# Kernel tuning notes

Hardware: AMD Instinct MI355X
Metric: run time of the kernel (lower is better)

The kernel has to match this reference:

```python
import jax, jax.numpy as jnp
import numpy as np

B, S, F, H, L = 128, 1024, 256, 256, 2


def setup_inputs() -> dict:
    key = jax.random.key(0)
    ks = jax.random.split(key, 6)
    x = jax.random.normal(ks[0], (B, S, F), dtype=jnp.float32)
    # nn.Linear default init ~ U(-1/sqrt(fan_in), 1/sqrt(fan_in)); use scaled normal for simplicity
    s_in = 1.0 / np.sqrt(F)
    s_h = 1.0 / np.sqrt(H)
    W_ih = jax.random.normal(ks[1], (L, 3 * H, F), dtype=jnp.float32) * s_in
    b_ih = jax.random.normal(ks[2], (L, 3 * H), dtype=jnp.float32) * s_in
    W_hh = jax.random.normal(ks[3], (L, 3 * H, H), dtype=jnp.float32) * s_h
    b_hh = jax.random.normal(ks[4], (L, 3 * H), dtype=jnp.float32) * s_h
    fw = jnp.ones((1, 1, F), dtype=jnp.float32)   # features_weighting (init: ones)
    tw = jnp.ones((1, S, 1), dtype=jnp.float32)   # times_weighting (init: ones)
    return {"x": x, "fw": fw, "tw": tw, "W_ih": W_ih, "b_ih": b_ih, "W_hh": W_hh, "b_hh": b_hh}


def _lstm_forward(x, fw, tw, W_ih, b_ih, W_hh, b_hh):
    batch = x.shape[0]
    xw = x * fw * tw  # (B,S,F)
    h0 = jnp.zeros((L, batch, H), dtype=x.dtype)
    c0 = jnp.zeros((L, batch, H), dtype=x.dtype)

    def step(carry, x_t):
        hs, cs = carry  # each (L,B,H)
        inp = x_t
        new_hs, new_cs = [], []
        for l in range(L):
            gates = inp @ W_ih[l].T + b_ih[l] + hs[l] @ W_hh[l].T + b_hh[l]  # (B,3H)
            i_g, g_g, o_g = jnp.split(gates, 3, axis=1)
            f = jax.nn.sigmoid(cs[l])            # NOTE: forget gate = sigmoid(c_prev) per source
            c = f * cs[l] + jax.nn.sigmoid(i_g) * jnp.tanh(g_g)
            h = jax.nn.sigmoid(o_g) * jnp.tanh(c)
            new_hs.append(h)
            new_cs.append(c)
            inp = h
        return (jnp.stack(new_hs), jnp.stack(new_cs)), inp

    (hs, cs), outs = jax.lax.scan(step, (h0, c0), jnp.swapaxes(xw, 0, 1))
    outputs = jnp.swapaxes(outs, 0, 1)  # (B,S,H)
    return outputs, hs, cs


def reference(x, fw, tw, W_ih, b_ih, W_hh, b_hh):
    return _lstm_forward(x, fw, tw, W_ih, b_ih, W_hh, b_hh)
```

## Files before the change

kernel.cpp:

```cpp
#include <hip/hip_runtime.h>
#include <math.h>

#define B_ 128
#define S_ 1024
#define F_ 256
#define H_ 256
#define G3 768
#define BGROUPS 4
#define NBLK 256
#define NTHR 64
#define H0_DEPTH 8
#define H1_DEPTH 2

#define SLAB_U64 4096
#define H0_U64 (H0_DEPTH * BGROUPS * SLAB_U64)
#define H1_U64 (H1_DEPTH * BGROUPS * SLAB_U64)
#define WS_ZERO_BYTES (4096 + (size_t)(H0_U64 + H1_U64) * 8)

typedef __bf16 bf16x8 __attribute__((ext_vector_type(8)));
typedef float f32x4 __attribute__((ext_vector_type(4)));
typedef unsigned short us8 __attribute__((ext_vector_type(8)));
typedef unsigned long long u64;

__device__ __forceinline__ float sigf(float v) { return 1.0f / (1.0f + __expf(-v)); }
__device__ __forceinline__ float tanh_fast(float v) {
    return __builtin_fmaf(2.0f, sigf(2.0f * v), -1.0f);
}
__device__ __forceinline__ unsigned short f2bf(float f) {
    unsigned u = __builtin_bit_cast(unsigned, f);
    return (unsigned short)((u + 0x7fffu + ((u >> 16) & 1u)) >> 16);
}
__device__ __forceinline__ f32x4 MF(bf16x8 a, bf16x8 b, f32x4 c) {
    return __builtin_amdgcn_mfma_f32_16x16x32_bf16(a, b, c, 0, 0, 0);
}
__device__ __forceinline__ u64 aload(const u64* p) {
    return __hip_atomic_load(p, __ATOMIC_RELAXED, __HIP_MEMORY_SCOPE_AGENT);
}
__device__ __forceinline__ void astore(u64* p, u64 v) {
    __hip_atomic_store(p, v, __ATOMIC_RELAXED, __HIP_MEMORY_SCOPE_AGENT);
}
__device__ __forceinline__ unsigned aload32(const unsigned* p) {
    return __hip_atomic_load(p, __ATOMIC_RELAXED, __HIP_MEMORY_SCOPE_AGENT);
}
__device__ __forceinline__ void astore32(unsigned* p, unsigned v) {
    __hip_atomic_store(p, v, __ATOMIC_RELAXED, __HIP_MEMORY_SCOPE_AGENT);
}

__device__ __forceinline__ void loadq(const u64* rdb, u64* q) {
    #pragma unroll
    for (int pl = 0; pl < 8; ++pl)
        #pragma unroll
        for (int jp = 0; jp < 4; ++jp)
            q[pl * 4 + jp] = aload(rdb + pl * 256 + jp * 16);
}
__device__ __forceinline__ bool tagok(const u64* q, unsigned tag) {
    unsigned acc = 0;
    #pragma unroll
    for (int i = 0; i < 32; ++i) {
        acc |= ((unsigned)q[i] ^ tag) & 0xFFFFu;
        acc |= ((unsigned)(q[i] >> 32) ^ tag) & 0xFFFFu;
    }
    return acc == 0u;
}
__device__ __forceinline__ bf16x8 unpk(const u64* qq) {
    us8 u;
    u[0] = (unsigned short)(qq[0] >> 16); u[1] = (unsigned short)(qq[0] >> 48);
    u[2] = (unsigned short)(qq[1] >> 16); u[3] = (unsigned short)(qq[1] >> 48);
    u[4] = (unsigned short)(qq[2] >> 16); u[5] = (unsigned short)(qq[2] >> 48);
    u[6] = (unsigned short)(qq[3] >> 16); u[7] = (unsigned short)(qq[3] >> 48);
    return __builtin_bit_cast(bf16x8, u);
}

__global__ __launch_bounds__(NTHR)
void lstm_w1(const float* __restrict__ x,
             const float* __restrict__ fw,
             const float* __restrict__ tw,
             const float* __restrict__ Wih,
             const float* __restrict__ bih,
             const float* __restrict__ Whh,
             const float* __restrict__ bhh,
             float* __restrict__ out,
             void* __restrict__ ws)
{
    __shared__ unsigned short sW[3 * 16 * 64 * 8];

    unsigned* prog = (unsigned*)ws;
    u64* h0buf = (u64*)((char*)ws + 4096);
    u64* h1buf = h0buf + H0_U64;
    float* outputs = out;
    float* hs = out + (size_t)B_ * S_ * H_;
    float* cs = hs + (size_t)2 * B_ * H_;

    const int bid   = blockIdx.x;
    const int lane  = threadIdx.x;
    const int ntw   = bid & 1;
    const int uh    = (bid >> 1) & 1;
    const int bg    = (bid >> 2) & 3;
    const int ug    = (bid >> 4) & 7;
    const int layer = (bid >> 7) & 1;

    const float* Wih_l = Wih + (size_t)layer * G3 * F_;
    const float* Whh_l = Whh + (size_t)layer * G3 * H_;

    for (int idx = lane; idx < 3 * 16 * 64; idx += NTHR) {
        const int l  = idx & 63;
        const int kt = (idx >> 6) & 15;
        const int g  = idx >> 10;
        const int grow = g * H_ + ug * 32 + uh * 16 + (l & 15);
        const int k = kt * 32 + (l >> 4) * 8;
        float4 a, b;
        if (k < 256) {
            const float* s = Wih_l + (size_t)grow * F_ + k;
            a = *(const float4*)s; b = *(const float4*)(s + 4);
            if (layer == 0) {
                const float4 wa = *(const float4*)(fw + k);
                const float4 wb = *(const float4*)(fw + k + 4);
                a.x *= wa.x; a.y *= wa.y; a.z *= wa.z; a.w *= wa.w;
                b.x *= wb.x; b.y *= wb.y; b.z *= wb.z; b.w *= wb.w;
            }
        } else {
            const float* s = Whh_l + (size_t)grow * H_ + (k - 256);
            a = *(const float4*)s; b = *(const float4*)(s + 4);
        }
        us8 w;
        w[0] = f2bf(a.x); w[1] = f2bf(a.y); w[2] = f2bf(a.z); w[3] = f2bf(a.w);
        w[4] = f2bf(b.x); w[5] = f2bf(b.y); w[6] = f2bf(b.z); w[7] = f2bf(b.w);
        *(us8*)&sW[(size_t)idx * 8] = w;
    }
    __syncthreads();

    float bia[3][4];
    #pragma unroll
    for (int r = 0; r < 4; ++r) {
        const int gu = ug * 32 + uh * 16 + (lane >> 4) * 4 + r;
        #pragma unroll
        for (int s = 0; s < 3; ++s)
            bia[s][r] = bih[layer * G3 + s * H_ + gu] + bhh[layer * G3 + s * H_ + gu];
    }

    const int ul0  = uh * 16 + (lane >> 4) * 4;
    const int hg0  = ug * 32 + ul0;
    const int bcol = bg * 32 + ntw * 16 + (lane & 15);
    const size_t wofs = (size_t)ntw * 2048 + (size_t)ug * 256
                      + (size_t)(uh * 2 + ((lane >> 4) >> 1)) * 64
                      + (size_t)(((lane >> 4) & 1) * 2) * 16 + (lane & 15);
    const size_t rofs = (size_t)ntw * 2048 + (size_t)(lane >> 4) * 64 + (lane & 15);
    const int dom = bg * 2 + ntw;

    float c_reg[4] = {0.f, 0.f, 0.f, 0.f};

    #define WAf(g, kt) (*(const bf16x8*)&sW[(size_t)(((g) * 16 + (kt)) * 64 + lane) * 8])

    if (layer == 0) {
        float4 xf[16];
        #pragma unroll
        for (int kt = 0; kt < 8; ++kt) {
            const float* s = x + ((size_t)bcol * S_ + 0) * F_ + kt * 32 + (lane >> 4) * 8;
            xf[2 * kt] = *(const float4*)s; xf[2 * kt + 1] = *(const float4*)(s + 4);
        }
        float twc = tw[0], twn = tw[1];

        for (int p = 0; p < S_; ++p) {
            const u64* rdb = h0buf + (size_t)(((p - 1) & 7) * BGROUPS + bg) * SLAB_U64 + rofs;
            u64 q[32];
            loadq(rdb, q);

            bf16x8 xb[8];
            #pragma unroll
            for (int kt = 0; kt < 8; ++kt) {
                const float4 a = xf[2 * kt], b = xf[2 * kt + 1];
                us8 w;
                w[0] = f2bf(a.x); w[1] = f2bf(a.y); w[2] = f2bf(a.z); w[3] = f2bf(a.w);
                w[4] = f2bf(b.x); w[5] = f2bf(b.y); w[6] = f2bf(b.z); w[7] = f2bf(b.w);
                xb[kt] = __builtin_bit_cast(bf16x8, w);
            }
            if (p + 1 < S_) {
                #pragma unroll
                for (int kt = 0; kt < 8; ++kt) {
                    const float* s = x + ((size_t)bcol * S_ + (p + 1)) * F_
                                   + kt * 32 + (lane >> 4) * 8;
                    xf[2 * kt] = *(const float4*)s; xf[2 * kt + 1] = *(const float4*)(s + 4);
                }
            }

            f32x4 ai = {0.f, 0.f, 0.f, 0.f}, ag = ai, ao = ai;
            #pragma unroll
            for (int kt = 0; kt < 8; ++kt) {
                ai = MF(WAf(0, kt), xb[kt], ai);
                ag = MF(WAf(1, kt), xb[kt], ag);
                ao = MF(WAf(2, kt), xb[kt], ao);
            }
            #pragma unroll
            for (int r = 0; r < 4; ++r) {
                ai[r] *= twc; ag[r] *= twc; ao[r] *= twc;
            }

            while (!__all(tagok(q, (unsigned)p))) loadq(rdb, q);
            #pragma unroll
            for (int pl = 0; pl < 8; ++pl) {
                const bf16x8 hb = unpk(&q[pl * 4]);
                ai = MF(WAf(0, 8 + pl), hb, ai);
                ag = MF(WAf(1, 8 + pl), hb, ag);
                ao = MF(WAf(2, 8 + pl), hb, ao);
            }

            if (p >= H0_DEPTH) {
                const unsigned need = (unsigned)(p - (H0_DEPTH - 1));
                bool ok;
                do {
                    const unsigned pv = (lane < 16)
                        ? aload32(&prog[dom * 16 + lane]) : need;
                    ok = __all((int)(pv >= need));
                } while (!ok);
            }

            u64* wb = h0buf + (size_t)((p & 7) * BGROUPS + bg) * SLAB_U64 + wofs;
            const unsigned tagv = (unsigned)(p + 1);
            float hnv[4], cnv[4];
            unsigned er[4];
            #pragma unroll
            for (int r = 0; r < 4; ++r) {
                const float gi = ai[r] + bia[0][r];
                const float gg = ag[r] + bia[1][r];
                const float go = ao[r] + bia[2][r];
                const float cp = c_reg[r];
                const float fg = sigf(cp);
                const float cn = fg * cp + sigf(gi) * tanh_fast(gg);
                const float hn = sigf(go) * tanh_fast(cn);
                c_reg[r] = cn; hnv[r] = hn; cnv[r] = cn;
                er[r] = ((unsigned)f2bf(hn) << 16) | tagv;
            }
            astore(wb,      er[0] | ((u64)er[1] << 32));
            astore(wb + 16, er[2] | ((u64)er[3] << 32));

            if (p == S_ - 1) {
                *(float4*)(hs + (size_t)bcol * H_ + hg0) =
                    make_float4(hnv[0], hnv[1], hnv[2], hnv[3]);
                *(float4*)(cs + (size_t)bcol * H_ + hg0) =
                    make_float4(cnv[0], cnv[1], cnv[2], cnv[3]);
            }
            twc = twn;
            if (p + 2 < S_) twn = tw[p + 2];
        }
    } else {
        for (int p = 1; p <= S_; ++p) {
            const int t = p - 1;
            const u64* rd0 = h0buf + (size_t)(((p - 1) & 7) * BGROUPS + bg) * SLAB_U64 + rofs;
            const u64* rd1 = h1buf + (size_t)(((p - 2) & 1) * BGROUPS + bg) * SLAB_U64 + rofs;
            u64 q0[32], q1[32];
            loadq(rd0, q0);
            loadq(rd1, q1);

            while (!__all(tagok(q0, (unsigned)p))) loadq(rd0, q0);
            if (lane == 0)
                astore32(&prog[dom * 16 + ug * 2 + uh], (unsigned)p);

            f32x4 ai = {0.f, 0.f, 0.f, 0.f}, ag = ai, ao = ai;
            #pragma unroll
            for (int pl = 0; pl < 8; ++pl) {
                const bf16x8 hb = unpk(&q0[pl * 4]);
                ai = MF(WAf(0, pl), hb, ai);
                ag = MF(WAf(1, pl), hb, ag);
                ao = MF(WAf(2, pl), hb, ao);
            }

            while (!__all(tagok(q1, (unsigned)(p - 1)))) loadq(rd1, q1);
            #pragma unroll
            for (int pl = 0; pl < 8; ++pl) {
                const bf16x8 hb = unpk(&q1[pl * 4]);
                ai = MF(WAf(0, 8 + pl), hb, ai);
                ag = MF(WAf(1, 8 + pl), hb, ag);
                ao = MF(WAf(2, 8 + pl), hb, ao);
            }

            u64* wb = h1buf + (size_t)(((p - 1) & 1) * BGROUPS + bg) * SLAB_U64 + wofs;
            const unsigned tagv = (unsigned)p;
            float hnv[4], cnv[4];
            unsigned er[4];
            #pragma unroll
            for (int r = 0; r < 4; ++r) {
                const float gi = ai[r] + bia[0][r];
                const float gg = ag[r] + bia[1][r];
                const float go = ao[r] + bia[2][r];
                const float cp = c_reg[r];
                const float fg = sigf(cp);
                const float cn = fg * cp + sigf(gi) * tanh_fast(gg);
                const float hn = sigf(go) * tanh_fast(cn);
                c_reg[r] = cn; hnv[r] = hn; cnv[r] = cn;
                er[r] = ((unsigned)f2bf(hn) << 16) | tagv;
            }
            astore(wb,      er[0] | ((u64)er[1] << 32));
            astore(wb + 16, er[2] | ((u64)er[3] << 32));

            *(float4*)(outputs + ((size_t)bcol * S_ + t) * H_ + hg0) =
                make_float4(hnv[0], hnv[1], hnv[2], hnv[3]);
            if (p == S_) {
                *(float4*)(hs + (size_t)B_ * H_ + (size_t)bcol * H_ + hg0) =
                    make_float4(hnv[0], hnv[1], hnv[2], hnv[3]);
                *(float4*)(cs + (size_t)B_ * H_ + (size_t)bcol * H_ + hg0) =
                    make_float4(cnv[0], cnv[1], cnv[2], cnv[3]);
            }
        }
    }
}

extern "C" void kernel_launch(void* const* d_in, const int* in_sizes, int n_in,
                              void* d_out, int out_size, void* d_ws, size_t ws_size,
                              hipStream_t stream) {
    const float* x   = (const float*)d_in[0];
    const float* fw  = (const float*)d_in[1];
    const float* tw  = (const float*)d_in[2];
    const float* Wih = (const float*)d_in[3];
    const float* bih = (const float*)d_in[4];
    const float* Whh = (const float*)d_in[5];
    const float* bhh = (const float*)d_in[6];
    float* out = (float*)d_out;

    hipMemsetAsync(d_ws, 0, WS_ZERO_BYTES, stream);

    void* kargs[] = { (void*)&x, (void*)&fw, (void*)&tw, (void*)&Wih, (void*)&bih,
                      (void*)&Whh, (void*)&bhh, (void*)&out, (void*)&d_ws };
    hipError_t e = hipLaunchCooperativeKernel((const void*)lstm_w1,
                                              dim3(NBLK), dim3(NTHR),
                                              kargs, 0, stream);
    if (e != hipSuccess) {
        lstm_w1<<<dim3(NBLK), dim3(NTHR), 0, stream>>>(
            x, fw, tw, Wih, bih, Whh, bhh, out, d_ws);
    }
}
```

Measured before the change: 4.004 ms.

## Halve block count; each block handles two batch groups with interleaved pipelines

The kernel now launches half as many single-wave blocks, and each block processes two batch groups. It interleaves their recurrent steps so one group's work can hide the other's wait on the handoff buffers. The next step's h-buffer reads are also prefetched right after the current step's stores, and s_sleep is added inside the spin loops to ease polling pressure. In exchange, each wave carries more register state (two copies of q and x) and does serial work per step, which could lengthen the critical path of the recurrence.

```diff
diff --git a/kernel.cpp b/kernel.cpp
--- a/kernel.cpp
+++ b/kernel.cpp
@@ -7,7 +7,7 @@
 #define H_ 256
 #define G3 768
 #define BGROUPS 4
-#define NBLK 256
+#define NBLK 128
 #define NTHR 64
 #define H0_DEPTH 8
 #define H1_DEPTH 2
@@ -71,8 +71,8 @@
     return __builtin_bit_cast(bf16x8, u);
 }
 
-__global__ __launch_bounds__(NTHR)
-void lstm_w1(const float* __restrict__ x,
+__global__ __launch_bounds__(NTHR, 1)
+void lstm_w2(const float* __restrict__ x,
              const float* __restrict__ fw,
              const float* __restrict__ tw,
              const float* __restrict__ Wih,
@@ -93,11 +93,11 @@
 
     const int bid   = blockIdx.x;
     const int lane  = threadIdx.x;
-    const int ntw   = bid & 1;
-    const int uh    = (bid >> 1) & 1;
-    const int bg    = (bid >> 2) & 3;
-    const int ug    = (bid >> 4) & 7;
-    const int layer = (bid >> 7) & 1;
+    const int bgp   = bid & 1;
+    const int nt    = (bid >> 1) & 1;
+    const int uh    = (bid >> 2) & 1;
+    const int ug    = (bid >> 3) & 7;
+    const int layer = (bid >> 6) & 1;
 
     const float* Wih_l = Wih + (size_t)layer * G3 * F_;
     const float* Whh_l = Whh + (size_t)layer * G3 * H_;
@@ -138,167 +138,200 @@
             bia[s][r] = bih[layer * G3 + s * H_ + gu] + bhh[layer * G3 + s * H_ + gu];
     }
 
-    const int ul0  = uh * 16 + (lane >> 4) * 4;
-    const int hg0  = ug * 32 + ul0;
-    const int bcol = bg * 32 + ntw * 16 + (lane & 15);
-    const size_t wofs = (size_t)ntw * 2048 + (size_t)ug * 256
+    const int ul0 = uh * 16 + (lane >> 4) * 4;
+    const int hg0 = ug * 32 + ul0;
+    const size_t wofs = (size_t)nt * 2048 + (size_t)ug * 256
                       + (size_t)(uh * 2 + ((lane >> 4) >> 1)) * 64
                       + (size_t)(((lane >> 4) & 1) * 2) * 16 + (lane & 15);
-    const size_t rofs = (size_t)ntw * 2048 + (size_t)(lane >> 4) * 64 + (lane & 15);
-    const int dom = bg * 2 + ntw;
-
-    float c_reg[4] = {0.f, 0.f, 0.f, 0.f};
+    const size_t rofs = (size_t)nt * 2048 + (size_t)(lane >> 4) * 64 + (lane & 15);
+
+    int bg[2], bcol[2], dom[2];
+    #pragma unroll
+    for (int c = 0; c < 2; ++c) {
+        bg[c]   = bgp * 2 + c;
+        bcol[c] = bg[c] * 32 + nt * 16 + (lane & 15);
+        dom[c]  = bg[c] * 2 + nt;
+    }
+
+    float c_reg[2][4] = {{0.f,0.f,0.f,0.f},{0.f,0.f,0.f,0.f}};
 
     #define WAf(g, kt) (*(const bf16x8*)&sW[(size_t)(((g) * 16 + (kt)) * 64 + lane) * 8])
 
     if (layer == 0) {
-        float4 xf[16];
+        float4 xr[2][16];
+        u64 q[2][32];
         #pragma unroll
-        for (int kt = 0; kt < 8; ++kt) {
-            const float* s = x + ((size_t)bcol * S_ + 0) * F_ + kt * 32 + (lane >> 4) * 8;
-            xf[2 * kt] = *(const float4*)s; xf[2 * kt + 1] = *(const float4*)(s + 4);
-        }
-        float twc = tw[0], twn = tw[1];
-
-        for (int p = 0; p < S_; ++p) {
-            const u64* rdb = h0buf + (size_t)(((p - 1) & 7) * BGROUPS + bg) * SLAB_U64 + rofs;
-            u64 q[32];
-            loadq(rdb, q);
-
-            bf16x8 xb[8];
+        for (int c = 0; c < 2; ++c) {
             #pragma unroll
             for (int kt = 0; kt < 8; ++kt) {
-                const float4 a = xf[2 * kt], b = xf[2 * kt + 1];
-                us8 w;
-                w[0] = f2bf(a.x); w[1] = f2bf(a.y); w[2] = f2bf(a.z); w[3] = f2bf(a.w);
-                w[4] = f2bf(b.x); w[5] = f2bf(b.y); w[6] = f2bf(b.z); w[7] = f2bf(b.w);
-                xb[kt] = __builtin_bit_cast(bf16x8, w);
+                const float* s = x + ((size_t)bcol[c] * S_) * F_ + kt * 32 + (lane >> 4) * 8;
+                xr[c][2 * kt] = *(const float4*)s;
+                xr[c][2 * kt + 1] = *(const float4*)(s + 4);
             }
-            if (p + 1 < S_) {
+            loadq(h0buf + (size_t)(7 * BGROUPS + bg[c]) * SLAB_U64 + rofs, q[c]);
+        }
+
+        for (int p = 0; p < S_; ++p) {
+            const float twc = tw[p];
+            #pragma unroll
+            for (int c = 0; c < 2; ++c) {
+                bf16x8 xb[8];
                 #pragma unroll
                 for (int kt = 0; kt < 8; ++kt) {
-                    const float* s = x + ((size_t)bcol * S_ + (p + 1)) * F_
-                                   + kt * 32 + (lane >> 4) * 8;
-                    xf[2 * kt] = *(const float4*)s; xf[2 * kt + 1] = *(const float4*)(s + 4);
+                    const float4 a = xr[c][2 * kt], b = xr[c][2 * kt + 1];
+                    us8 w;
+                    w[0] = f2bf(a.x); w[1] = f2bf(a.y); w[2] = f2bf(a.z); w[3] = f2bf(a.w);
+                    w[4] = f2bf(b.x); w[5] = f2bf(b.y); w[6] = f2bf(b.z); w[7] = f2bf(b.w);
+                    xb[kt] = __builtin_bit_cast(bf16x8, w);
+                }
+                f32x4 ai = {0.f, 0.f, 0.f, 0.f}, ag = ai, ao = ai;
+                #pragma unroll
+                for (int kt = 0; kt < 8; ++kt) {
+                    ai = MF(WAf(0, kt), xb[kt], ai);
+                    ag = MF(WAf(1, kt), xb[kt], ag);
+                    ao = MF(WAf(2, kt), xb[kt], ao);
+                }
+                #pragma unroll
+                for (int r = 0; r < 4; ++r) { ai[r] *= twc; ag[r] *= twc; ao[r] *= twc; }
+
+                const u64* rdb = h0buf
+                    + (size_t)(((p - 1) & 7) * BGROUPS + bg[c]) * SLAB_U64 + rofs;
+                while (!__all(tagok(q[c], (unsigned)p))) {
+                    __builtin_amdgcn_s_sleep(1);
+                    loadq(rdb, q[c]);
+                }
+                #pragma unroll
+                for (int pl = 0; pl < 8; ++pl) {
+                    const bf16x8 hb = unpk(&q[c][pl * 4]);
+                    ai = MF(WAf(0, 8 + pl), hb, ai);
+                    ag = MF(WAf(1, 8 + pl), hb, ag);
+                    ao = MF(WAf(2, 8 + pl), hb, ao);
+                }
+
+                if (p >= H0_DEPTH) {
+                    const unsigned need = (unsigned)(p - (H0_DEPTH - 1));
+                    bool ok;
+                    do {
+                        const unsigned pv = (lane < 16)
+                            ? aload32(&prog[dom[c] * 16 + lane]) : need;
+                        ok = __all((int)(pv >= need));
+                    } while (!ok);
+                }
+
+                u64* wb = h0buf + (size_t)((p & 7) * BGROUPS + bg[c]) * SLAB_U64 + wofs;
+                const unsigned tagv = (unsigned)(p + 1);
+                float hnv[4], cnv[4];
+                unsigned er[4];
+                #pragma unroll
+                for (int r = 0; r < 4; ++r) {
+                    const float gi = ai[r] + bia[0][r];
+                    const float gg = ag[r] + bia[1][r];
+                    const float go = ao[r] + bia[2][r];
+                    const float cp = c_reg[c][r];
+                    const float fg = sigf(cp);
+                    const float cn = fg * cp + sigf(gi) * tanh_fast(gg);
+                    const float hn = sigf(go) * tanh_fast(cn);
+                    c_reg[c][r] = cn; hnv[r] = hn; cnv[r] = cn;
+                    er[r] = ((unsigned)f2bf(hn) << 16) | tagv;
+                }
+                astore(wb,      er[0] | ((u64)er[1] << 32));
+                astore(wb + 16, er[2] | ((u64)er[3] << 32));
+
+                if (p == S_ - 1) {
+                    *(float4*)(hs + (size_t)bcol[c] * H_ + hg0) =
+                        make_float4(hnv[0], hnv[1], hnv[2], hnv[3]);
+                    *(float4*)(cs + (size_t)bcol[c] * H_ + hg0) =
+                        make_float4(cnv[0], cnv[1], cnv[2], cnv[3]);
+                } else {
+                    #pragma unroll
+                    for (int kt = 0; kt < 8; ++kt) {
+                        const float* s = x + ((size_t)bcol[c] * S_ + (p + 1)) * F_
+                                       + kt * 32 + (lane >> 4) * 8;
+                        xr[c][2 * kt] = *(const float4*)s;
+                        xr[c][2 * kt + 1] = *(const float4*)(s + 4);
+                    }
+                    loadq(h0buf + (size_t)((p & 7) * BGROUPS + bg[c]) * SLAB_U64 + rofs,
+                          q[c]);
                 }
             }
-
-            f32x4 ai = {0.f, 0.f, 0.f, 0.f}, ag = ai, ao = ai;
-            #pragma unroll
-            for (int kt = 0; kt < 8; ++kt) {
-                ai = MF(WAf(0, kt), xb[kt], ai);
-                ag = MF(WAf(1, kt), xb[kt], ag);
-                ao = MF(WAf(2, kt), xb[kt], ao);
-            }
-            #pragma unroll
-            for (int r = 0; r < 4; ++r) {
-                ai[r] *= twc; ag[r] *= twc; ao[r] *= twc;
-            }
-
-            while (!__all(tagok(q, (unsigned)p))) loadq(rdb, q);
-            #pragma unroll
-            for (int pl = 0; pl < 8; ++pl) {
-                const bf16x8 hb = unpk(&q[pl * 4]);
-                ai = MF(WAf(0, 8 + pl), hb, ai);
-                ag = MF(WAf(1, 8 + pl), hb, ag);
-                ao = MF(WAf(2, 8 + pl), hb, ao);
-            }
-
-            if (p >= H0_DEPTH) {
-                const unsigned need = (unsigned)(p - (H0_DEPTH - 1));
-                bool ok;
-                do {
-                    const unsigned pv = (lane < 16)
-                        ? aload32(&prog[dom * 16 + lane]) : need;
-                    ok = __all((int)(pv >= need));
-                } while (!ok);
-            }
-
-            u64* wb = h0buf + (size_t)((p & 7) * BGROUPS + bg) * SLAB_U64 + wofs;
-            const unsigned tagv = (unsigned)(p + 1);
-            float hnv[4], cnv[4];
-            unsigned er[4];
-            #pragma unroll
-            for (int r = 0; r < 4; ++r) {
-                const float gi = ai[r] + bia[0][r];
-                const float gg = ag[r] + bia[1][r];
-                const float go = ao[r] + bia[2][r];
-                const float cp = c_reg[r];
-                const float fg = sigf(cp);
-                const float cn = fg * cp + sigf(gi) * tanh_fast(gg);
-                const float hn = sigf(go) * tanh_fast(cn);
-                c_reg[r] = cn; hnv[r] = hn; cnv[r] = cn;
-                er[r] = ((unsigned)f2bf(hn) << 16) | tagv;
-            }
-            astore(wb,      er[0] | ((u64)er[1] << 32));
-            astore(wb + 16, er[2] | ((u64)er[3] << 32));
-
-            if (p == S_ - 1) {
-                *(float4*)(hs + (size_t)bcol * H_ + hg0) =
-                    make_float4(hnv[0], hnv[1], hnv[2], hnv[3]);
-                *(float4*)(cs + (size_t)bcol * H_ + hg0) =
-                    make_float4(cnv[0], cnv[1], cnv[2], cnv[3]);
-            }
-            twc = twn;
-            if (p + 2 < S_) twn = tw[p + 2];
         }
     } else {
+        u64 q0[2][32], q1[2][32];
+        #pragma unroll
+        for (int c = 0; c < 2; ++c) {
+            loadq(h0buf + (size_t)(0 * BGROUPS + bg[c]) * SLAB_U64 + rofs, q0[c]);
+            loadq(h1buf + (size_t)(1 * BGROUPS + bg[c]) * SLAB_U64 + rofs, q1[c]);
+        }
+
         for (int p = 1; p <= S_; ++p) {
             const int t = p - 1;
-            const u64* rd0 = h0buf + (size_t)(((p - 1) & 7) * BGROUPS + bg) * SLAB_U64 + rofs;
-            const u64* rd1 = h1buf + (size_t)(((p - 2) & 1) * BGROUPS + bg) * SLAB_U64 + rofs;
-            u64 q0[32], q1[32];
-            loadq(rd0, q0);
-            loadq(rd1, q1);
-
-            while (!__all(tagok(q0, (unsigned)p))) loadq(rd0, q0);
-            if (lane == 0)
-                astore32(&prog[dom * 16 + ug * 2 + uh], (unsigned)p);
-
-            f32x4 ai = {0.f, 0.f, 0.f, 0.f}, ag = ai, ao = ai;
             #pragma unroll
-            for (int pl = 0; pl < 8; ++pl) {
-                const bf16x8 hb = unpk(&q0[pl * 4]);
-                ai = MF(WAf(0, pl), hb, ai);
-                ag = MF(WAf(1, pl), hb, ag);
-                ao = MF(WAf(2, pl), hb, ao);
-            }
-
-            while (!__all(tagok(q1, (unsigned)(p - 1)))) loadq(rd1, q1);
-            #pragma unroll
-            for (int pl = 0; pl < 8; ++pl) {
-                const bf16x8 hb = unpk(&q1[pl * 4]);
-                ai = MF(WAf(0, 8 + pl), hb, ai);
-                ag = MF(WAf(1, 8 + pl), hb, ag);
-                ao = MF(WAf(2, 8 + pl), hb, ao);
-            }
-
-            u64* wb = h1buf + (size_t)(((p - 1) & 1) * BGROUPS + bg) * SLAB_U64 + wofs;
-            const unsigned tagv = (unsigned)p;
-            float hnv[4], cnv[4];
-            unsigned er[4];
-            #pragma unroll
-            for (int r = 0; r < 4; ++r) {
-                const float gi = ai[r] + bia[0][r];
-                const float gg = ag[r] + bia[1][r];
-                const float go = ao[r] + bia[2][r];
-                const float cp = c_reg[r];
-                const float fg = sigf(cp);
-                const float cn = fg * cp + sigf(gi) * tanh_fast(gg);
-                const float hn = sigf(go) * tanh_fast(cn);
-                c_reg[r] = cn; hnv[r] = hn; cnv[r] = cn;
-                er[r] = ((unsigned)f2bf(hn) << 16) | tagv;
-            }
-            astore(wb,      er[0] | ((u64)er[1] << 32));
-            astore(wb + 16, er[2] | ((u64)er[3] << 32));
-
-            *(float4*)(outputs + ((size_t)bcol * S_ + t) * H_ + hg0) =
-                make_float4(hnv[0], hnv[1], hnv[2], hnv[3]);
-            if (p == S_) {
-                *(float4*)(hs + (size_t)B_ * H_ + (size_t)bcol * H_ + hg0) =
+            for (int c = 0; c < 2; ++c) {
+                const u64* rd0 = h0buf
+                    + (size_t)(((p - 1) & 7) * BGROUPS + bg[c]) * SLAB_U64 + rofs;
+                while (!__all(tagok(q0[c], (unsigned)p))) {
+                    __builtin_amdgcn_s_sleep(1);
+                    loadq(rd0, q0[c]);
+                }
+                if (lane == 0)
+                    astore32(&prog[dom[c] * 16 + ug * 2 + uh], (unsigned)p);
+
+                f32x4 ai = {0.f, 0.f, 0.f, 0.f}, ag = ai, ao = ai;
+                #pragma unroll
+                for (int pl = 0; pl < 8; ++pl) {
+                    const bf16x8 hb = unpk(&q0[c][pl * 4]);
+                    ai = MF(WAf(0, pl), hb, ai);
+                    ag = MF(WAf(1, pl), hb, ag);
+                    ao = MF(WAf(2, pl), hb, ao);
+                }
+
+                const u64* rd1 = h1buf
+                    + (size_t)(((p - 2) & 1) * BGROUPS + bg[c]) * SLAB_U64 + rofs;
+                while (!__all(tagok(q1[c], (unsigned)(p - 1)))) {
+                    __builtin_amdgcn_s_sleep(1);
+                    loadq(rd1, q1[c]);
+                }
+                #pragma unroll
+                for (int pl = 0; pl < 8; ++pl) {
+                    const bf16x8 hb = unpk(&q1[c][pl * 4]);
+                    ai = MF(WAf(0, 8 + pl), hb, ai);
+                    ag = MF(WAf(1, 8 + pl), hb, ag);
+                    ao = MF(WAf(2, 8 + pl), hb, ao);
+                }
+
+                u64* wb = h1buf
+                    + (size_t)(((p - 1) & 1) * BGROUPS + bg[c]) * SLAB_U64 + wofs;
+                const unsigned tagv = (unsigned)p;
+                float hnv[4], cnv[4];
+                unsigned er[4];
+                #pragma unroll
+                for (int r = 0; r < 4; ++r) {
+                    const float gi = ai[r] + bia[0][r];
+                    const float gg = ag[r] + bia[1][r];
+                    const float go = ao[r] + bia[2][r];
+                    const float cp = c_reg[c][r];
+                    const float fg = sigf(cp);
+                    const float cn = fg * cp + sigf(gi) * tanh_fast(gg);
+                    const float hn = sigf(go) * tanh_fast(cn);
+                    c_reg[c][r] = cn; hnv[r] = hn; cnv[r] = cn;
+                    er[r] = ((unsigned)f2bf(hn) << 16) | tagv;
+                }
+                astore(wb,      er[0] | ((u64)er[1] << 32));
+                astore(wb + 16, er[2] | ((u64)er[3] << 32));
+
+                *(float4*)(outputs + ((size_t)bcol[c] * S_ + t) * H_ + hg0) =
                     make_float4(hnv[0], hnv[1], hnv[2], hnv[3]);
-                *(float4*)(cs + (size_t)B_ * H_ + (size_t)bcol * H_ + hg0) =
-                    make_float4(cnv[0], cnv[1], cnv[2], cnv[3]);
+                if (p == S_) {
+                    *(float4*)(hs + (size_t)B_ * H_ + (size_t)bcol[c] * H_ + hg0) =
+                        make_float4(hnv[0], hnv[1], hnv[2], hnv[3]);
+                    *(float4*)(cs + (size_t)B_ * H_ + (size_t)bcol[c] * H_ + hg0) =
+                        make_float4(cnv[0], cnv[1], cnv[2], cnv[3]);
+                } else {
+                    loadq(h0buf + (size_t)((p & 7) * BGROUPS + bg[c]) * SLAB_U64 + rofs,
+                          q0[c]);
+                    loadq(h1buf + (size_t)(((p - 1) & 1) * BGROUPS + bg[c]) * SLAB_U64 + rofs,
+                          q1[c]);
+                }
             }
         }
     }
@@ -320,11 +353,11 @@
 
     void* kargs[] = { (void*)&x, (void*)&fw, (void*)&tw, (void*)&Wih, (void*)&bih,
                       (void*)&Whh, (void*)&bhh, (void*)&out, (void*)&d_ws };
-    hipError_t e = hipLaunchCooperativeKernel((const void*)lstm_w1,
+    hipError_t e = hipLaunchCooperativeKernel((const void*)lstm_w2,
                                               dim3(NBLK), dim3(NTHR),
                                               kargs, 0, stream);
     if (e != hipSuccess) {
-        lstm_w1<<<dim3(NBLK), dim3(NTHR), 0, stream>>>(
+        lstm_w2<<<dim3(NBLK), dim3(NTHR), 0, stream>>>(
             x, fw, tw, Wih, bih, Whh, bhh, out, d_ws);
     }
 }
```

New measurement: 10.35 ms. 2.59x slower.

## Deepen layer-0 ring, software-pipeline input projection and h prefetch

Applied to the files above, without the earlier changes.

Enlarges the layer-0 hidden-state ring from 8 to 32 slots so layer 0 can run further ahead of layer 1 before stalling on progress counters. Moves the next step's input-projection MFMAs and x loads after the current step's state publish, and issues the next h-slab load speculatively at the end of each iteration so polling starts with data in flight. Caches the minimum consumer progress and reduces it with shuffles to avoid polling every step. This costs more workspace memory and more live registers, and the speculative loads may return stale tags and need a re-poll.

```diff
diff --git a/kernel.cpp b/kernel.cpp
--- a/kernel.cpp
+++ b/kernel.cpp
@@ -9,7 +9,7 @@
 #define BGROUPS 4
 #define NBLK 256
 #define NTHR 64
-#define H0_DEPTH 8
+#define H0_DEPTH 32
 #define H1_DEPTH 2
 
 #define SLAB_U64 4096
@@ -72,7 +72,7 @@
 }
 
 __global__ __launch_bounds__(NTHR)
-void lstm_w1(const float* __restrict__ x,
+void lstm_w3(const float* __restrict__ x,
              const float* __restrict__ fw,
              const float* __restrict__ tw,
              const float* __restrict__ Wih,
@@ -152,50 +152,50 @@
     #define WAf(g, kt) (*(const bf16x8*)&sW[(size_t)(((g) * 16 + (kt)) * 64 + lane) * 8])
 
     if (layer == 0) {
-        float4 xf[16];
+        float4 xr[16];
+        u64 q[32];
+        f32x4 ai, ag, ao;
+
         #pragma unroll
         for (int kt = 0; kt < 8; ++kt) {
-            const float* s = x + ((size_t)bcol * S_ + 0) * F_ + kt * 32 + (lane >> 4) * 8;
-            xf[2 * kt] = *(const float4*)s; xf[2 * kt + 1] = *(const float4*)(s + 4);
-        }
-        float twc = tw[0], twn = tw[1];
-
-        for (int p = 0; p < S_; ++p) {
-            const u64* rdb = h0buf + (size_t)(((p - 1) & 7) * BGROUPS + bg) * SLAB_U64 + rofs;
-            u64 q[32];
-            loadq(rdb, q);
-
+            const float* s = x + ((size_t)bcol * S_) * F_ + kt * 32 + (lane >> 4) * 8;
+            xr[2 * kt] = *(const float4*)s; xr[2 * kt + 1] = *(const float4*)(s + 4);
+        }
+        {
             bf16x8 xb[8];
             #pragma unroll
             for (int kt = 0; kt < 8; ++kt) {
-                const float4 a = xf[2 * kt], b = xf[2 * kt + 1];
+                const float4 a = xr[2 * kt], b = xr[2 * kt + 1];
                 us8 w;
                 w[0] = f2bf(a.x); w[1] = f2bf(a.y); w[2] = f2bf(a.z); w[3] = f2bf(a.w);
                 w[4] = f2bf(b.x); w[5] = f2bf(b.y); w[6] = f2bf(b.z); w[7] = f2bf(b.w);
                 xb[kt] = __builtin_bit_cast(bf16x8, w);
             }
-            if (p + 1 < S_) {
-                #pragma unroll
-                for (int kt = 0; kt < 8; ++kt) {
-                    const float* s = x + ((size_t)bcol * S_ + (p + 1)) * F_
-                                   + kt * 32 + (lane >> 4) * 8;
-                    xf[2 * kt] = *(const float4*)s; xf[2 * kt + 1] = *(const float4*)(s + 4);
-                }
-            }
-
-            f32x4 ai = {0.f, 0.f, 0.f, 0.f}, ag = ai, ao = ai;
+            ai = f32x4{0.f,0.f,0.f,0.f}; ag = ai; ao = ai;
             #pragma unroll
             for (int kt = 0; kt < 8; ++kt) {
                 ai = MF(WAf(0, kt), xb[kt], ai);
                 ag = MF(WAf(1, kt), xb[kt], ag);
                 ao = MF(WAf(2, kt), xb[kt], ao);
             }
-            #pragma unroll
-            for (int r = 0; r < 4; ++r) {
-                ai[r] *= twc; ag[r] *= twc; ao[r] *= twc;
-            }
-
+            const float twc = tw[0];
+            #pragma unroll
+            for (int r = 0; r < 4; ++r) { ai[r] *= twc; ag[r] *= twc; ao[r] *= twc; }
+        }
+        #pragma unroll
+        for (int kt = 0; kt < 8; ++kt) {
+            const float* s = x + ((size_t)bcol * S_ + 1) * F_ + kt * 32 + (lane >> 4) * 8;
+            xr[2 * kt] = *(const float4*)s; xr[2 * kt + 1] = *(const float4*)(s + 4);
+        }
+        loadq(h0buf + (size_t)((H0_DEPTH - 1) * BGROUPS + bg) * SLAB_U64 + rofs, q);
+
+        unsigned prog_min = 0;
+
+        for (int p = 0; p < S_; ++p) {
+            const u64* rdb = h0buf
+                + (size_t)((((p - 1) & (H0_DEPTH - 1)) * BGROUPS) + bg) * SLAB_U64 + rofs;
             while (!__all(tagok(q, (unsigned)p))) loadq(rdb, q);
+
             #pragma unroll
             for (int pl = 0; pl < 8; ++pl) {
                 const bf16x8 hb = unpk(&q[pl * 4]);
@@ -204,17 +204,22 @@
                 ao = MF(WAf(2, 8 + pl), hb, ao);
             }
 
-            if (p >= H0_DEPTH) {
+            if (p >= H0_DEPTH && prog_min < (unsigned)(p - (H0_DEPTH - 1))) {
                 const unsigned need = (unsigned)(p - (H0_DEPTH - 1));
-                bool ok;
+                unsigned mv;
                 do {
-                    const unsigned pv = (lane < 16)
-                        ? aload32(&prog[dom * 16 + lane]) : need;
-                    ok = __all((int)(pv >= need));
-                } while (!ok);
-            }
-
-            u64* wb = h0buf + (size_t)((p & 7) * BGROUPS + bg) * SLAB_U64 + wofs;
+                    unsigned pv = (lane < 16)
+                        ? aload32(&prog[dom * 16 + lane]) : 0xFFFFFFFFu;
+                    #pragma unroll
+                    for (int o = 1; o < 16; o <<= 1)
+                        pv = min(pv, (unsigned)__shfl_xor((int)pv, o));
+                    mv = (unsigned)__shfl((int)pv, 0);
+                } while (mv < need);
+                prog_min = mv;
+            }
+
+            u64* wb = h0buf
+                + (size_t)(((p & (H0_DEPTH - 1)) * BGROUPS) + bg) * SLAB_U64 + wofs;
             const unsigned tagv = (unsigned)(p + 1);
             float hnv[4], cnv[4];
             unsigned er[4];
@@ -238,19 +243,48 @@
                     make_float4(hnv[0], hnv[1], hnv[2], hnv[3]);
                 *(float4*)(cs + (size_t)bcol * H_ + hg0) =
                     make_float4(cnv[0], cnv[1], cnv[2], cnv[3]);
-            }
-            twc = twn;
-            if (p + 2 < S_) twn = tw[p + 2];
+            } else {
+                bf16x8 xb[8];
+                #pragma unroll
+                for (int kt = 0; kt < 8; ++kt) {
+                    const float4 a = xr[2 * kt], b = xr[2 * kt + 1];
+                    us8 w;
+                    w[0] = f2bf(a.x); w[1] = f2bf(a.y); w[2] = f2bf(a.z); w[3] = f2bf(a.w);
+                    w[4] = f2bf(b.x); w[5] = f2bf(b.y); w[6] = f2bf(b.z); w[7] = f2bf(b.w);
+                    xb[kt] = __builtin_bit_cast(bf16x8, w);
+                }
+                ai = f32x4{0.f,0.f,0.f,0.f}; ag = ai; ao = ai;
+                #pragma unroll
+                for (int kt = 0; kt < 8; ++kt) {
+                    ai = MF(WAf(0, kt), xb[kt], ai);
+                    ag = MF(WAf(1, kt), xb[kt], ag);
+                    ao = MF(WAf(2, kt), xb[kt], ao);
+                }
+                const float twc = tw[p + 1];
+                #pragma unroll
+                for (int r = 0; r < 4; ++r) { ai[r] *= twc; ag[r] *= twc; ao[r] *= twc; }
+                if (p + 2 < S_) {
+                    #pragma unroll
+                    for (int kt = 0; kt < 8; ++kt) {
+                        const float* s = x + ((size_t)bcol * S_ + (p + 2)) * F_
+                                       + kt * 32 + (lane >> 4) * 8;
+                        xr[2 * kt] = *(const float4*)s;
+                        xr[2 * kt + 1] = *(const float4*)(s + 4);
+                    }
+                }
+                loadq(h0buf + (size_t)(((p & (H0_DEPTH - 1)) * BGROUPS) + bg) * SLAB_U64
+                      + rofs, q);
+            }
         }
     } else {
+        u64 q0[32], q1[32];
+        loadq(h0buf + (size_t)(0 * BGROUPS + bg) * SLAB_U64 + rofs, q0);
+        loadq(h1buf + (size_t)(1 * BGROUPS + bg) * SLAB_U64 + rofs, q1);
+
         for (int p = 1; p <= S_; ++p) {
             const int t = p - 1;
-            const u64* rd0 = h0buf + (size_t)(((p - 1) & 7) * BGROUPS + bg) * SLAB_U64 + rofs;
-            const u64* rd1 = h1buf + (size_t)(((p - 2) & 1) * BGROUPS + bg) * SLAB_U64 + rofs;
-            u64 q0[32], q1[32];
-            loadq(rd0, q0);
-            loadq(rd1, q1);
-
+            const u64* rd0 = h0buf
+                + (size_t)((((p - 1) & (H0_DEPTH - 1)) * BGROUPS) + bg) * SLAB_U64 + rofs;
             while (!__all(tagok(q0, (unsigned)p))) loadq(rd0, q0);
             if (lane == 0)
                 astore32(&prog[dom * 16 + ug * 2 + uh], (unsigned)p);
@@ -264,6 +298,8 @@
                 ao = MF(WAf(2, pl), hb, ao);
             }
 
+            const u64* rd1 = h1buf
+                + (size_t)((((p - 2) & 1) * BGROUPS) + bg) * SLAB_U64 + rofs;
             while (!__all(tagok(q1, (unsigned)(p - 1)))) loadq(rd1, q1);
             #pragma unroll
             for (int pl = 0; pl < 8; ++pl) {
@@ -273,7 +309,8 @@
                 ao = MF(WAf(2, 8 + pl), hb, ao);
             }
 
-            u64* wb = h1buf + (size_t)(((p - 1) & 1) * BGROUPS + bg) * SLAB_U64 + wofs;
+            u64* wb = h1buf
+                + (size_t)((((p - 1) & 1) * BGROUPS) + bg) * SLAB_U64 + wofs;
             const unsigned tagv = (unsigned)p;
             float hnv[4], cnv[4];
             unsigned er[4];
@@ -299,6 +336,11 @@
                     make_float4(hnv[0], hnv[1], hnv[2], hnv[3]);
                 *(float4*)(cs + (size_t)B_ * H_ + (size_t)bcol * H_ + hg0) =
                     make_float4(cnv[0], cnv[1], cnv[2], cnv[3]);
+            } else {
+                loadq(h0buf + (size_t)(((p & (H0_DEPTH - 1)) * BGROUPS) + bg) * SLAB_U64
+                      + rofs, q0);
+                loadq(h1buf + (size_t)((((p - 1) & 1) * BGROUPS) + bg) * SLAB_U64
+                      + rofs, q1);
             }
         }
     }
@@ -320,11 +362,11 @@
 
     void* kargs[] = { (void*)&x, (void*)&fw, (void*)&tw, (void*)&Wih, (void*)&bih,
                       (void*)&Whh, (void*)&bhh, (void*)&out, (void*)&d_ws };
-    hipError_t e = hipLaunchCooperativeKernel((const void*)lstm_w1,
+    hipError_t e = hipLaunchCooperativeKernel((const void*)lstm_w3,
                                               dim3(NBLK), dim3(NTHR),
                                               kargs, 0, stream);
     if (e != hipSuccess) {
-        lstm_w1<<<dim3(NBLK), dim3(NTHR), 0, stream>>>(
+        lstm_w3<<<dim3(NBLK), dim3(NTHR), 0, stream>>>(
             x, fw, tw, Wih, bih, Whh, bhh, out, d_ws);
     }
 }
```

After: 8.811 ms. 2.2x slower.
